# Kernel optimization log

Hardware: AMD Instinct MI355X
Metric: run time of the kernel (lower is better)

Reference implementation:

```python
import jax, jax.numpy as jnp
import numpy as np

DIM = 768
HEADS = 12
HIDDEN = 3072
EPS = 1e-5


def _layernorm(x, g, b):
    mu = jnp.mean(x, axis=-1, keepdims=True)
    var = jnp.var(x, axis=-1, keepdims=True)
    return (x - mu) * jax.lax.rsqrt(var + EPS) * g + b


def setup_inputs() -> dict:
    key = jax.random.key(0)
    ks = jax.random.split(key, 10)
    s_in = 1.0 / np.sqrt(DIM)
    s_hid = 1.0 / np.sqrt(HIDDEN)
    return {
        "x": jax.random.normal(ks[0], (8, 1024, DIM), dtype=jnp.float32),
        "ln1_g": jnp.ones((DIM,), jnp.float32),
        "ln1_b": jnp.zeros((DIM,), jnp.float32),
        "qkv_w": jax.random.uniform(ks[1], (DIM, 3 * DIM), jnp.float32, -s_in, s_in),
        "qkv_b": jnp.zeros((3 * DIM,), jnp.float32),
        "proj_w": jax.random.uniform(ks[2], (DIM, DIM), jnp.float32, -s_in, s_in),
        "proj_b": jnp.zeros((DIM,), jnp.float32),
        "ln2_g": jnp.ones((DIM,), jnp.float32),
        "ln2_b": jnp.zeros((DIM,), jnp.float32),
        "fc1_w": jax.random.uniform(ks[3], (DIM, HIDDEN), jnp.float32, -s_in, s_in),
        "fc1_b": jnp.zeros((HIDDEN,), jnp.float32),
        "fc2_w": jax.random.uniform(ks[4], (HIDDEN, DIM), jnp.float32, -s_hid, s_hid),
        "fc2_b": jnp.zeros((DIM,), jnp.float32),
    }


def reference(x, ln1_g, ln1_b, qkv_w, qkv_b, proj_w, proj_b,
              ln2_g, ln2_b, fc1_w, fc1_b, fc2_w, fc2_b):
    B, N, C = x.shape
    H = HEADS
    Dh = C // H
    scale = Dh ** -0.5

    # --- attention sublayer (pre-norm) ---
    h = _layernorm(x, ln1_g, ln1_b)
    qkv = h @ qkv_w + qkv_b  # [B,N,3C]
    qkv = qkv.reshape(B, N, 3, H, Dh)
    q = qkv[:, :, 0].transpose(0, 2, 1, 3)  # [B,H,N,Dh]
    k = qkv[:, :, 1].transpose(0, 2, 1, 3)
    v = qkv[:, :, 2].transpose(0, 2, 1, 3)
    attn = jax.nn.softmax(jnp.einsum('bhnd,bhmd->bhnm', q, k) * scale, axis=-1)
    o = jnp.einsum('bhnm,bhmd->bhnd', attn, v)  # [B,H,N,Dh]
    o = o.transpose(0, 2, 1, 3).reshape(B, N, C)
    x = x + (o @ proj_w + proj_b)

    # --- MLP sublayer (pre-norm) ---
    h = _layernorm(x, ln2_g, ln2_b)
    h = jax.nn.gelu(h @ fc1_w + fc1_b, approximate=False)
    x = x + (h @ fc2_w + fc2_b)
    return x
```

## Files before the change

### kernel.cpp

```cpp
#include <hip/hip_runtime.h>
#include <math.h>

#define DIM    768
#define HEADS  12
#define HIDDEN 3072
#define SEQ    1024
#define NTOK   8192
#define QKVLD  2304

typedef __bf16 bf16_t;
typedef __bf16 bf16x4 __attribute__((ext_vector_type(4)));
typedef __bf16 bf16x8 __attribute__((ext_vector_type(8)));
typedef float  f32x4  __attribute__((ext_vector_type(4)));

union ABFrag { bf16x4 h[2]; bf16x8 v; };

__device__ __forceinline__ void gload16(const void* g, void* l) {
  __builtin_amdgcn_global_load_lds(
      (const __attribute__((address_space(1))) void*)g,
      (__attribute__((address_space(3))) void*)l, 16, 0, 0);
}

__device__ __forceinline__ f32x4 mfma16(bf16x8 a, bf16x8 b, f32x4 c) {
  return __builtin_amdgcn_mfma_f32_16x16x32_bf16(a, b, c, 0, 0, 0);
}

__device__ __forceinline__ bf16x8 ldsfrag(const bf16_t* base, int row, int lc) {
  return *(const bf16x8*)(base + row * 64 + ((lc ^ (row & 7)) << 3));
}

__device__ __forceinline__ float gelu_f(float v) {
  float u = v * fmaf(v * v, 0.0356774081f, 0.7978845608f);
  u = fminf(u, 15.0f);
  float t = __builtin_amdgcn_exp2f(u * 2.8853900817779268f);
  return v * t * __builtin_amdgcn_rcpf(t + 1.0f);
}

__global__ __launch_bounds__(256) void ln_kernel(
    const float* __restrict__ x, const float* __restrict__ gw,
    const float* __restrict__ bw, bf16_t* __restrict__ out) {
  const int row = blockIdx.x * 4 + (threadIdx.x >> 6);
  const int lane = threadIdx.x & 63;
  const float* xr = x + (size_t)row * DIM;
  f32x4 v[3];
  float s = 0.f, s2 = 0.f;
  #pragma unroll
  for (int i = 0; i < 3; ++i) {
    v[i] = *(const f32x4*)(xr + lane * 4 + i * 256);
    #pragma unroll
    for (int j = 0; j < 4; ++j) { s += v[i][j]; s2 += v[i][j] * v[i][j]; }
  }
  #pragma unroll
  for (int o = 32; o > 0; o >>= 1) {
    s += __shfl_xor(s, o);
    s2 += __shfl_xor(s2, o);
  }
  const float mu  = s * (1.0f / DIM);
  const float var = s2 * (1.0f / DIM) - mu * mu;
  const float rs  = rsqrtf(var + 1e-5f);
  bf16_t* orow = out + (size_t)row * DIM;
  #pragma unroll
  for (int i = 0; i < 3; ++i) {
    const int c = lane * 4 + i * 256;
    f32x4 gv = *(const f32x4*)(gw + c);
    f32x4 bv = *(const f32x4*)(bw + c);
    bf16x4 o4;
    #pragma unroll
    for (int j = 0; j < 4; ++j)
      o4[j] = (bf16_t)((v[i][j] - mu) * rs * gv[j] + bv[j]);
    *(bf16x4*)(orow + c) = o4;
  }
}

struct WT4 {
  const float* W0; const float* W1; const float* W2; const float* W3;
  bf16_t* T0; bf16_t* T1; bf16_t* T2; bf16_t* T3;
};
__global__ __launch_bounds__(256) void wtrans4_kernel(WT4 p) {
  __shared__ float tile[32][33];
  const int bid = blockIdx.x;
  const float* W; bf16_t* Wt; int K, N, nx, lb;
  if (bid < 1728)      { W = p.W0; Wt = p.T0; K = 768;  N = 2304; nx = 72; lb = bid; }
  else if (bid < 2304) { W = p.W1; Wt = p.T1; K = 768;  N = 768;  nx = 24; lb = bid - 1728; }
  else if (bid < 4608) { W = p.W2; Wt = p.T2; K = 768;  N = 3072; nx = 96; lb = bid - 2304; }
  else                 { W = p.W3; Wt = p.T3; K = 3072; N = 768;  nx = 24; lb = bid - 4608; }
  const int bx = lb % nx, by = lb / nx;
  const int tx = threadIdx.x & 31, ty = threadIdx.x >> 5;
  const int n0 = bx * 32, k0 = by * 32;
  #pragma unroll
  for (int i = 0; i < 4; ++i)
    tile[ty + i * 8][tx] = W[(size_t)(k0 + ty + i * 8) * N + n0 + tx];
  __syncthreads();
  #pragma unroll
  for (int i = 0; i < 4; ++i)
    Wt[(size_t)(n0 + ty + i * 8) * K + k0 + tx] = (bf16_t)tile[tx][ty + i * 8];
}

__global__ __launch_bounds__(256) void vtrans_kernel(
    const bf16_t* __restrict__ qkv, bf16_t* __restrict__ vt) {
  __shared__ bf16_t tile[64][68];
  const int bh = blockIdx.y, b = bh / HEADS, h = bh % HEADS;
  const int n0 = blockIdx.x * 64;
  const int t = threadIdx.x;
  const int c = t & 15, r0 = t >> 4;
  const bf16_t* src = qkv + (size_t)(b * SEQ + n0) * QKVLD + 2 * DIM + h * 64;
  #pragma unroll
  for (int i = 0; i < 4; ++i) {
    const int n = r0 + i * 16;
    bf16x4 v4 = *(const bf16x4*)(src + (size_t)n * QKVLD + c * 4);
    #pragma unroll
    for (int j = 0; j < 4; ++j) tile[c * 4 + j][n] = v4[j];
  }
  __syncthreads();
  bf16_t* dst = vt + (size_t)bh * 64 * SEQ + n0;
  #pragma unroll
  for (int i = 0; i < 4; ++i) {
    const int d = r0 + i * 16;
    *(bf16x4*)(dst + (size_t)d * SEQ + c * 4) = *(const bf16x4*)(&tile[d][c * 4]);
  }
}

template <int MODE>
__global__ __launch_bounds__(256) void gemm_sb(
    const bf16_t* __restrict__ A, const bf16_t* __restrict__ Bt,
    int N, int K,
    const float* __restrict__ bias, const float* __restrict__ res,
    void* __restrict__ outv, int gx) {
  __shared__ bf16_t sA[128 * 64];
  __shared__ bf16_t sB[128 * 64];
  const int tid = threadIdx.x;
  const int lane = tid & 63;
  const int wid = tid >> 6;
  const int g = lane >> 4, r16 = lane & 15;

  const int nwg = gridDim.x;
  const int cpx = nwg >> 3;
  const int sw = (blockIdx.x & 7) * cpx + (blockIdx.x >> 3);
  const int bx = sw % gx, by = sw / gx;
  const int row0 = by * 128, col0 = bx * 128;
  const int wr = (wid >> 1) * 64, wc = (wid & 1) * 64;

  f32x4 acc[4][4];
  #pragma unroll
  for (int m = 0; m < 4; ++m)
    #pragma unroll
    for (int n = 0; n < 4; ++n) acc[m][n] = f32x4{0.f, 0.f, 0.f, 0.f};

  const int kSteps = K >> 6;
  for (int kt = 0; kt < kSteps; ++kt) {
    __syncthreads();
    #pragma unroll
    for (int rnd = 0; rnd < 4; ++rnd) {
      const int c = rnd * 256 + tid;
      const int row = c >> 3, scp = (c & 7) ^ (row & 7);
      gload16(A + (size_t)(row0 + row) * K + (size_t)kt * 64 + scp * 8, &sA[c * 8]);
    }
    #pragma unroll
    for (int rnd = 0; rnd < 4; ++rnd) {
      const int c = rnd * 256 + tid;
      const int row = c >> 3, scp = (c & 7) ^ (row & 7);
      gload16(Bt + (size_t)(col0 + row) * K + (size_t)kt * 64 + scp * 8, &sB[c * 8]);
    }
    __syncthreads();
    bf16x8 af[4][2], bfr[4][2];
    #pragma unroll
    for (int m = 0; m < 4; ++m)
      #pragma unroll
      for (int kk = 0; kk < 2; ++kk)
        af[m][kk] = ldsfrag(sA, wr + m * 16 + r16, kk * 4 + g);
    #pragma unroll
    for (int n = 0; n < 4; ++n)
      #pragma unroll
      for (int kk = 0; kk < 2; ++kk)
        bfr[n][kk] = ldsfrag(sB, wc + n * 16 + r16, kk * 4 + g);
    #pragma unroll
    for (int kk = 0; kk < 2; ++kk)
      #pragma unroll
      for (int m = 0; m < 4; ++m)
        #pragma unroll
        for (int n = 0; n < 4; ++n)
          acc[m][n] = mfma16(af[m][kk], bfr[n][kk], acc[m][n]);
  }

  #pragma unroll
  for (int m = 0; m < 4; ++m) {
    const int rowb = row0 + wr + m * 16 + 4 * g;
    #pragma unroll
    for (int n = 0; n < 4; ++n) {
      const int col = col0 + wc + n * 16 + r16;
      const float bv = bias[col];
      #pragma unroll
      for (int r = 0; r < 4; ++r) {
        const size_t idx = (size_t)(rowb + r) * N + col;
        float v = acc[m][n][r] + bv;
        if (MODE == 0) {
          ((bf16_t*)outv)[idx] = (bf16_t)v;
        } else if (MODE == 1) {
          ((float*)outv)[idx] = v + res[idx];
        } else {
          ((bf16_t*)outv)[idx] = (bf16_t)gelu_f(v);
        }
      }
    }
  }
}

template <int MODE, int BN>
__global__ __launch_bounds__(256) void gemm_db(
    const bf16_t* __restrict__ A, const bf16_t* __restrict__ Bt,
    int N, int K,
    const float* __restrict__ bias, const float* __restrict__ res,
    void* __restrict__ outv, int gx) {
  constexpr int WAVES_N = (BN == 128) ? 2 : 1;
  constexpr int WM = (BN == 128) ? 4 : 2;
  constexpr int WN = 4;
  __shared__ bf16_t sA[2][128 * 64];
  __shared__ bf16_t sB[2][BN * 64];
  const int tid = threadIdx.x;
  const int lane = tid & 63;
  const int wid = tid >> 6;
  const int g = lane >> 4, r16 = lane & 15;

  const int nwg = gridDim.x;
  const int cpx = nwg >> 3;
  const int sw = (blockIdx.x & 7) * cpx + (blockIdx.x >> 3);
  const int bx = sw % gx, by = sw / gx;
  const int row0 = by * 128, col0 = bx * BN;
  const int wr = (wid / WAVES_N) * (WM * 16);
  const int wc = (wid % WAVES_N) * (WN * 16);

  auto stage = [&](int p, int kt) {
    #pragma unroll
    for (int rnd = 0; rnd < 4; ++rnd) {
      const int c = rnd * 256 + tid;
      const int row = c >> 3, scp = (c & 7) ^ (row & 7);
      gload16(A + (size_t)(row0 + row) * K + (size_t)kt * 64 + scp * 8,
              &sA[p][c * 8]);
    }
    #pragma unroll
    for (int rnd = 0; rnd < BN / 32; ++rnd) {
      const int c = rnd * 256 + tid;
      const int row = c >> 3, scp = (c & 7) ^ (row & 7);
      gload16(Bt + (size_t)(col0 + row) * K + (size_t)kt * 64 + scp * 8,
              &sB[p][c * 8]);
    }
  };

  f32x4 acc[WM][WN];
  #pragma unroll
  for (int m = 0; m < WM; ++m)
    #pragma unroll
    for (int n = 0; n < WN; ++n) acc[m][n] = f32x4{0.f, 0.f, 0.f, 0.f};

  const int kSteps = K >> 6;
  stage(0, 0);
  for (int kt = 0; kt < kSteps; ++kt) {
    const int cur = kt & 1;
    __syncthreads();
    if (kt + 1 < kSteps) stage(cur ^ 1, kt + 1);

    bf16x8 af[WM][2], bfr[WN][2];
    #pragma unroll
    for (int m = 0; m < WM; ++m)
      #pragma unroll
      for (int kk = 0; kk < 2; ++kk)
        af[m][kk] = ldsfrag(&sA[cur][0], wr + m * 16 + r16, kk * 4 + g);
    #pragma unroll
    for (int n = 0; n < WN; ++n)
      #pragma unroll
      for (int kk = 0; kk < 2; ++kk)
        bfr[n][kk] = ldsfrag(&sB[cur][0], wc + n * 16 + r16, kk * 4 + g);
    #pragma unroll
    for (int kk = 0; kk < 2; ++kk)
      #pragma unroll
      for (int m = 0; m < WM; ++m)
        #pragma unroll
        for (int n = 0; n < WN; ++n)
          acc[m][n] = mfma16(af[m][kk], bfr[n][kk], acc[m][n]);
  }

  #pragma unroll
  for (int m = 0; m < WM; ++m) {
    const int rowb = row0 + wr + m * 16 + 4 * g;
    #pragma unroll
    for (int n = 0; n < WN; ++n) {
      const int col = col0 + wc + n * 16 + r16;
      const float bv = bias[col];
      #pragma unroll
      for (int r = 0; r < 4; ++r) {
        const size_t idx = (size_t)(rowb + r) * N + col;
        float v = acc[m][n][r] + bv;
        if (MODE == 0) {
          ((bf16_t*)outv)[idx] = (bf16_t)v;
        } else if (MODE == 1) {
          ((float*)outv)[idx] = v + res[idx];
        } else {
          ((bf16_t*)outv)[idx] = (bf16_t)gelu_f(v);
        }
      }
    }
  }
}

__global__ __launch_bounds__(512) void attn_kernel(
    const bf16_t* __restrict__ qkv, const bf16_t* __restrict__ vt,
    bf16_t* __restrict__ o) {
  __shared__ bf16_t kbuf[2][64 * 64];
  __shared__ bf16_t vbuf[2][64 * 64];
  const int bh = blockIdx.x, b = bh / HEADS, h = bh % HEADS;
  const int q0 = blockIdx.y * 128;
  const int tid = threadIdx.x, lane = tid & 63, wid = tid >> 6;
  const int g = lane >> 4, r16 = lane & 15;

  const bf16_t* qptr = qkv + (size_t)b * SEQ * QKVLD + h * 64;
  const bf16_t* kptr = qptr + DIM;
  const bf16_t* vtp  = vt + (size_t)bh * 64 * SEQ;

  bf16x8 aq[2];
  {
    const bf16_t* qr = qptr + (size_t)(q0 + wid * 16 + r16) * QKVLD;
    aq[0] = *(const bf16x8*)(qr + 8 * g);
    aq[1] = *(const bf16x8*)(qr + 32 + 8 * g);
  }

  int koff[4][2];
  int voff[4][2][2];
  #pragma unroll
  for (int i = 0; i < 4; ++i) {
    const int row = i * 16 + r16, s = row & 7, rp = row * 64;
    #pragma unroll
    for (int e2 = 0; e2 < 2; ++e2) {
      koff[i][e2] = rp + (((4 * e2 + g) ^ s) << 3);
      const int o0 = e2 * 32 + 4 * g, o1 = o0 + 16;
      voff[i][e2][0] = rp + ((((o0 >> 3) ^ s) << 3) | (o0 & 7));
      voff[i][e2][1] = rp + ((((o1 >> 3) ^ s) << 3) | (o1 & 7));
    }
  }

  float lacc = 0.f;
  f32x4 acco[4];
  #pragma unroll
  for (int n = 0; n < 4; ++n) acco[n] = f32x4{0.f, 0.f, 0.f, 0.f};

  const int srow = tid >> 3, sscp = (tid & 7) ^ (srow & 7);
  const bf16_t* kSrc = kptr + (size_t)srow * QKVLD + sscp * 8;
  const bf16_t* vSrc = vtp + (size_t)srow * SEQ + sscp * 8;
  auto stage = [&](int buf, int kv0) {
    gload16(kSrc + (size_t)kv0 * QKVLD, &kbuf[buf][tid * 8]);
    gload16(vSrc + kv0, &vbuf[buf][tid * 8]);
  };

  const float C2 = 0.125f * 1.4426950408889634f;

  stage(0, 0);
  for (int it = 0; it < SEQ / 64; ++it) {
    const int cur = it & 1;
    __syncthreads();
    if (it + 1 < SEQ / 64) stage(cur ^ 1, (it + 1) * 64);
    const bf16_t* kb = kbuf[cur];
    const bf16_t* vb = vbuf[cur];

    f32x4 st[4];
    __builtin_amdgcn_s_setprio(1);
    #pragma unroll
    for (int t = 0; t < 4; ++t) {
      st[t] = f32x4{0.f, 0.f, 0.f, 0.f};
      st[t] = mfma16(*(const bf16x8*)(kb + koff[t][0]), aq[0], st[t]);
      st[t] = mfma16(*(const bf16x8*)(kb + koff[t][1]), aq[1], st[t]);
    }
    __builtin_amdgcn_s_setprio(0);

    float p[4][4];
    #pragma unroll
    for (int t = 0; t < 4; ++t)
      #pragma unroll
      for (int r = 0; r < 4; ++r) {
        float e = __builtin_amdgcn_exp2f(fmaf(st[t][r], C2, -16.0f));
        p[t][r] = e;
        lacc += e;
      }

    ABFrag pa0, pa1;
    #pragma unroll
    for (int r = 0; r < 4; ++r) {
      pa0.h[0][r] = (bf16_t)p[0][r];
      pa0.h[1][r] = (bf16_t)p[1][r];
      pa1.h[0][r] = (bf16_t)p[2][r];
      pa1.h[1][r] = (bf16_t)p[3][r];
    }

    __builtin_amdgcn_s_setprio(1);
    #pragma unroll
    for (int n = 0; n < 4; ++n) {
      ABFrag bv0, bv1;
      bv0.h[0] = *(const bf16x4*)(vb + voff[n][0][0]);
      bv0.h[1] = *(const bf16x4*)(vb + voff[n][0][1]);
      acco[n] = mfma16(pa0.v, bv0.v, acco[n]);
      bv1.h[0] = *(const bf16x4*)(vb + voff[n][1][0]);
      bv1.h[1] = *(const bf16x4*)(vb + voff[n][1][1]);
      acco[n] = mfma16(pa1.v, bv1.v, acco[n]);
    }
    __builtin_amdgcn_s_setprio(0);
  }

  float lt = lacc;
  lt += __shfl_xor(lt, 16);
  lt += __shfl_xor(lt, 32);
  float linv[4];
  #pragma unroll
  for (int r = 0; r < 4; ++r) linv[r] = 1.0f / __shfl(lt, 4 * g + r);
  bf16_t* op = o + (size_t)(b * SEQ + q0 + wid * 16 + 4 * g) * DIM + h * 64;
  #pragma unroll
  for (int n = 0; n < 4; ++n)
    #pragma unroll
    for (int r = 0; r < 4; ++r)
      op[(size_t)r * DIM + n * 16 + r16] = (bf16_t)(acco[n][r] * linv[r]);
}

extern "C" void kernel_launch(void* const* d_in, const int* in_sizes, int n_in,
                              void* d_out, int out_size, void* d_ws, size_t ws_size,
                              hipStream_t stream) {
  const float* x      = (const float*)d_in[0];
  const float* ln1_g  = (const float*)d_in[1];
  const float* ln1_b  = (const float*)d_in[2];
  const float* qkv_w  = (const float*)d_in[3];
  const float* qkv_b  = (const float*)d_in[4];
  const float* proj_w = (const float*)d_in[5];
  const float* proj_b = (const float*)d_in[6];
  const float* ln2_g  = (const float*)d_in[7];
  const float* ln2_b  = (const float*)d_in[8];
  const float* fc1_w  = (const float*)d_in[9];
  const float* fc1_b  = (const float*)d_in[10];
  const float* fc2_w  = (const float*)d_in[11];
  const float* fc2_b  = (const float*)d_in[12];
  float* out = (float*)d_out;

  char* ws = (char*)d_ws;
  size_t off = 0;
  auto alloc = [&](size_t bytes) -> void* {
    void* p = ws + off;
    off += (bytes + 255) & ~(size_t)255;
    return p;
  };
  bf16_t* wqkvT  = (bf16_t*)alloc((size_t)QKVLD * DIM * 2);
  bf16_t* wprojT = (bf16_t*)alloc((size_t)DIM * DIM * 2);
  bf16_t* wfc1T  = (bf16_t*)alloc((size_t)HIDDEN * DIM * 2);
  bf16_t* wfc2T  = (bf16_t*)alloc((size_t)DIM * HIDDEN * 2);
  bf16_t* buf1   = (bf16_t*)alloc((size_t)NTOK * DIM * 2);
  bf16_t* buf2   = (bf16_t*)alloc((size_t)NTOK * HIDDEN * 2);
  bf16_t* buf3   = (bf16_t*)alloc((size_t)NTOK * DIM * 2);
  float*  x1     = (float*)alloc((size_t)NTOK * DIM * 4);

  bf16_t* h1 = buf1;     bf16_t* obf = buf1;
  bf16_t* qkvbf = buf2;  bf16_t* h3 = buf2;
  bf16_t* vt = buf3;     bf16_t* h2 = buf3;
  (void)in_sizes; (void)n_in; (void)out_size; (void)ws_size;

  WT4 wp;
  wp.W0 = qkv_w;  wp.T0 = wqkvT;
  wp.W1 = proj_w; wp.T1 = wprojT;
  wp.W2 = fc1_w;  wp.T2 = wfc1T;
  wp.W3 = fc2_w;  wp.T3 = wfc2T;
  wtrans4_kernel<<<6912, 256, 0, stream>>>(wp);

  ln_kernel<<<NTOK / 4, 256, 0, stream>>>(x, ln1_g, ln1_b, h1);
  gemm_sb<0><<<(QKVLD / 128) * (NTOK / 128), 256, 0, stream>>>(
      h1, wqkvT, QKVLD, DIM, qkv_b, nullptr, qkvbf, QKVLD / 128);
  vtrans_kernel<<<dim3(SEQ / 64, 8 * HEADS), 256, 0, stream>>>(qkvbf, vt);
  attn_kernel<<<dim3(8 * HEADS, SEQ / 128), 512, 0, stream>>>(qkvbf, vt, obf);
  gemm_db<1, 64><<<(DIM / 64) * (NTOK / 128), 256, 0, stream>>>(
      obf, wprojT, DIM, DIM, proj_b, x, x1, DIM / 64);
  ln_kernel<<<NTOK / 4, 256, 0, stream>>>(x1, ln2_g, ln2_b, h2);
  gemm_sb<2><<<(HIDDEN / 128) * (NTOK / 128), 256, 0, stream>>>(
      h2, wfc1T, HIDDEN, DIM, fc1_b, nullptr, h3, HIDDEN / 128);
  gemm_db<1, 64><<<(DIM / 64) * (NTOK / 128), 256, 0, stream>>>(
      h3, wfc2T, DIM, HIDDEN, fc2_b, x1, out, DIM / 64);
}
```

Measured before the change: 221.8 us.

## Double-buffer QKV and FC1 GEMM LDS tiles with K-step of 32

Replaces the single-buffered 128x128 GEMM used for QKV and FC1 with a double-buffered version. The next K-slice loads into the alternate LDS buffer while MFMAs run on the current one, which halves the barriers per step and hides global-load latency. The K step shrinks from 64 to 32 so two buffers fit in the same LDS footprint, with a new XOR swizzle for 32-wide rows. The trade-off is twice as many loop iterations, with less MFMA work per barrier.

```diff
diff --git a/kernel.cpp b/kernel.cpp
--- a/kernel.cpp
+++ b/kernel.cpp
@@ -27,6 +27,10 @@
 
 __device__ __forceinline__ bf16x8 ldsfrag(const bf16_t* base, int row, int lc) {
   return *(const bf16x8*)(base + row * 64 + ((lc ^ (row & 7)) << 3));
+}
+
+__device__ __forceinline__ bf16x8 ldsfrag32(const bf16_t* base, int row, int g) {
+  return *(const bf16x8*)(base + row * 32 + ((g ^ ((row >> 1) & 3)) << 3));
 }
 
 __device__ __forceinline__ float gelu_f(float v) {
@@ -121,13 +125,13 @@
 }
 
 template <int MODE>
-__global__ __launch_bounds__(256) void gemm_sb(
+__global__ __launch_bounds__(256) void gemm_db32(
     const bf16_t* __restrict__ A, const bf16_t* __restrict__ Bt,
     int N, int K,
     const float* __restrict__ bias, const float* __restrict__ res,
     void* __restrict__ outv, int gx) {
-  __shared__ bf16_t sA[128 * 64];
-  __shared__ bf16_t sB[128 * 64];
+  __shared__ bf16_t sA[2][128 * 32];
+  __shared__ bf16_t sB[2][128 * 32];
   const int tid = threadIdx.x;
   const int lane = tid & 63;
   const int wid = tid >> 6;
@@ -140,46 +144,46 @@
   const int row0 = by * 128, col0 = bx * 128;
   const int wr = (wid >> 1) * 64, wc = (wid & 1) * 64;
 
+  auto stage = [&](int p, int kt) {
+    #pragma unroll
+    for (int rnd = 0; rnd < 2; ++rnd) {
+      const int c = rnd * 256 + tid;
+      const int row = c >> 2, scp = (c & 3) ^ ((row >> 1) & 3);
+      gload16(A + (size_t)(row0 + row) * K + (size_t)kt * 32 + scp * 8,
+              &sA[p][c * 8]);
+    }
+    #pragma unroll
+    for (int rnd = 0; rnd < 2; ++rnd) {
+      const int c = rnd * 256 + tid;
+      const int row = c >> 2, scp = (c & 3) ^ ((row >> 1) & 3);
+      gload16(Bt + (size_t)(col0 + row) * K + (size_t)kt * 32 + scp * 8,
+              &sB[p][c * 8]);
+    }
+  };
+
   f32x4 acc[4][4];
   #pragma unroll
   for (int m = 0; m < 4; ++m)
     #pragma unroll
     for (int n = 0; n < 4; ++n) acc[m][n] = f32x4{0.f, 0.f, 0.f, 0.f};
 
-  const int kSteps = K >> 6;
+  const int kSteps = K >> 5;
+  stage(0, 0);
   for (int kt = 0; kt < kSteps; ++kt) {
+    const int cur = kt & 1;
     __syncthreads();
-    #pragma unroll
-    for (int rnd = 0; rnd < 4; ++rnd) {
-      const int c = rnd * 256 + tid;
-      const int row = c >> 3, scp = (c & 7) ^ (row & 7);
-      gload16(A + (size_t)(row0 + row) * K + (size_t)kt * 64 + scp * 8, &sA[c * 8]);
-    }
-    #pragma unroll
-    for (int rnd = 0; rnd < 4; ++rnd) {
-      const int c = rnd * 256 + tid;
-      const int row = c >> 3, scp = (c & 7) ^ (row & 7);
-      gload16(Bt + (size_t)(col0 + row) * K + (size_t)kt * 64 + scp * 8, &sB[c * 8]);
-    }
-    __syncthreads();
-    bf16x8 af[4][2], bfr[4][2];
+    if (kt + 1 < kSteps) stage(cur ^ 1, kt + 1);
+
+    bf16x8 af[4], bfr[4];
+    #pragma unroll
+    for (int m = 0; m < 4; ++m) af[m] = ldsfrag32(&sA[cur][0], wr + m * 16 + r16, g);
+    #pragma unroll
+    for (int n = 0; n < 4; ++n) bfr[n] = ldsfrag32(&sB[cur][0], wc + n * 16 + r16, g);
     #pragma unroll
     for (int m = 0; m < 4; ++m)
       #pragma unroll
-      for (int kk = 0; kk < 2; ++kk)
-        af[m][kk] = ldsfrag(sA, wr + m * 16 + r16, kk * 4 + g);
-    #pragma unroll
-    for (int n = 0; n < 4; ++n)
-      #pragma unroll
-      for (int kk = 0; kk < 2; ++kk)
-        bfr[n][kk] = ldsfrag(sB, wc + n * 16 + r16, kk * 4 + g);
-    #pragma unroll
-    for (int kk = 0; kk < 2; ++kk)
-      #pragma unroll
-      for (int m = 0; m < 4; ++m)
-        #pragma unroll
-        for (int n = 0; n < 4; ++n)
-          acc[m][n] = mfma16(af[m][kk], bfr[n][kk], acc[m][n]);
+      for (int n = 0; n < 4; ++n)
+        acc[m][n] = mfma16(af[m], bfr[n], acc[m][n]);
   }
 
   #pragma unroll
@@ -464,14 +468,14 @@
   wtrans4_kernel<<<6912, 256, 0, stream>>>(wp);
 
   ln_kernel<<<NTOK / 4, 256, 0, stream>>>(x, ln1_g, ln1_b, h1);
-  gemm_sb<0><<<(QKVLD / 128) * (NTOK / 128), 256, 0, stream>>>(
+  gemm_db32<0><<<(QKVLD / 128) * (NTOK / 128), 256, 0, stream>>>(
       h1, wqkvT, QKVLD, DIM, qkv_b, nullptr, qkvbf, QKVLD / 128);
   vtrans_kernel<<<dim3(SEQ / 64, 8 * HEADS), 256, 0, stream>>>(qkvbf, vt);
   attn_kernel<<<dim3(8 * HEADS, SEQ / 128), 512, 0, stream>>>(qkvbf, vt, obf);
   gemm_db<1, 64><<<(DIM / 64) * (NTOK / 128), 256, 0, stream>>>(
       obf, wprojT, DIM, DIM, proj_b, x, x1, DIM / 64);
   ln_kernel<<<NTOK / 4, 256, 0, stream>>>(x1, ln2_g, ln2_b, h2);
-  gemm_sb<2><<<(HIDDEN / 128) * (NTOK / 128), 256, 0, stream>>>(
+  gemm_db32<2><<<(HIDDEN / 128) * (NTOK / 128), 256, 0, stream>>>(
       h2, wfc1T, HIDDEN, DIM, fc1_b, nullptr, h3, HIDDEN / 128);
   gemm_db<1, 64><<<(DIM / 64) * (NTOK / 128), 256, 0, stream>>>(
       h3, wfc2T, DIM, HIDDEN, fc2_b, x1, out, DIM / 64);
```

Result: slower. 235.0 us (+6.0%).
